# Kernel tuning notes

Hardware: AMD Instinct MI355X
Metric: run time of the kernel (lower is better)

Reference implementation:

```python
import jax, jax.numpy as jnp
import numpy as np

HIDDEN = 2048
B, T, K = 64, 512, 49  # K = 7x7 spatial grid

def setup_inputs() -> dict:
    key = jax.random.key(0)
    ks = jax.random.split(key, 7)
    def xavier(k, shape):
        fan_in, fan_out = shape[1], shape[0]
        bound = float(np.sqrt(6.0 / (fan_in + fan_out)))
        return jax.random.uniform(k, shape, jnp.float32, -bound, bound)
    return {
        "V": jax.random.normal(ks[0], (B, K, HIDDEN), jnp.float32),
        "h_t": jax.random.normal(ks[1], (B, T, HIDDEN), jnp.float32),
        "sent_t": jax.random.normal(ks[2], (B, T, HIDDEN), jnp.float32),
        "Wv": xavier(ks[3], (K, HIDDEN)),
        "Wg": xavier(ks[4], (K, HIDDEN)),
        "Ws": xavier(ks[5], (K, HIDDEN)),
        "Wh": xavier(ks[6], (1, K)),
    }

def reference(V, h_t, sent_t, Wv, Wg, Ws, Wh):
    # Dropout is identity (eval mode / deterministic reference).
    wh = Wh[0]                                    # [K]
    pv = jnp.einsum('bkd,jd->bkj', V, Wv)         # [B,K,K]
    pg = jnp.einsum('btd,jd->btj', h_t, Wg)       # [B,T,K]
    content_v = pv[:, None, :, :] + pg[:, :, None, :]   # [B,T,K,K]
    z_t = jnp.tanh(content_v) @ wh                # [B,T,K]
    alpha_t = jax.nn.softmax(z_t, axis=-1)        # spatial attention
    c_t = jnp.einsum('btk,bkd->btd', alpha_t, V)  # [B,T,HIDDEN]
    content_s = jnp.einsum('btd,jd->btj', sent_t, Ws) + pg  # [B,T,K]
    z_ext = jnp.tanh(content_s) @ wh              # [B,T]
    extend = jnp.concatenate([z_t, z_ext[..., None]], axis=-1)  # [B,T,K+1]
    alpha_hat = jax.nn.softmax(extend, axis=-1)
    beta_t = alpha_hat[:, :, -1:]                 # sentinel gate [B,T,1]
    c_hat_t = beta_t * sent_t + (1.0 - beta_t) * c_t
    return (c_hat_t, alpha_t, beta_t)
```

## Files before the change

### kernel.cpp

```cpp
#include <hip/hip_runtime.h>

#define HIDDEN 2048
#define NB 64
#define NT 512
#define NK 49

typedef __attribute__((ext_vector_type(4))) float f32x4;
typedef __attribute__((ext_vector_type(8))) short short8;

__device__ __forceinline__ unsigned cvtpk_bf16(float a, float b) {
    unsigned r;
    asm("v_cvt_pk_bf16_f32 %0, %1, %2" : "=v"(r) : "v"(a), "v"(b));
    return r;
}

__device__ __forceinline__ unsigned short f2bf(float x) {
    union { float f; unsigned u; } v; v.f = x;
    unsigned r = v.u + 0x7FFF + ((v.u >> 16) & 1);
    return (unsigned short)(r >> 16);
}

__global__ __launch_bounds__(256) void convert_w(
    const float* __restrict__ Wg, const float* __restrict__ Ws,
    const float* __restrict__ Wv, unsigned short* __restrict__ Wf)
{
    int tau = blockIdx.x * 256 + threadIdx.x;
    int m   = tau >> 14;
    int rem = tau & 16383;
    int c   = rem >> 12;
    int s   = (rem >> 6) & 63;
    int l   = rem & 63;
    int col = c * 16 + (l & 15);
    int k0  = s * 32 + ((l >> 4) << 3);

    const float* W = (m == 0) ? Wg : (m == 1) ? Ws : Wv;
    unsigned short out[8];
    if (col < NK) {
        const float* p = W + (size_t)col * HIDDEN + k0;
        #pragma unroll
        for (int j = 0; j < 8; j++) out[j] = f2bf(p[j]);
    } else {
        #pragma unroll
        for (int j = 0; j < 8; j++) out[j] = 0;
    }
    unsigned short* dst = Wf + (size_t)tau * 8;
    #pragma unroll
    for (int j = 0; j < 8; j++) dst[j] = out[j];
}

__global__ __launch_bounds__(256) void gemm_mfma(
    const float* __restrict__ h, const float* __restrict__ s,
    const float* __restrict__ V, const unsigned short* __restrict__ Wf,
    float* __restrict__ pg, float* __restrict__ ps, float* __restrict__ pv)
{
    int w = threadIdx.x >> 6, lane = threadIdx.x & 63;
    int gw = blockIdx.x * 4 + w;

    const float* A; float* C; int rowBase; const unsigned short* wf;
    if (gw < 2048)      { A = h; C = pg; rowBase = gw * 16;          wf = Wf; }
    else if (gw < 4096) { A = s; C = ps; rowBase = (gw - 2048) * 16; wf = Wf + (size_t)16384 * 8; }
    else                { A = V; C = pv; rowBase = (gw - 4096) * 16; wf = Wf + (size_t)32768 * 8; }

    const float* ap = A + (size_t)(rowBase + (lane & 15)) * HIDDEN + ((lane >> 4) << 3);
    const short8* bp = (const short8*)(wf + (size_t)lane * 8);

    f32x4 acc0 = {0.f, 0.f, 0.f, 0.f};
    f32x4 acc1 = acc0, acc2 = acc0, acc3 = acc0;

    #pragma unroll 2
    for (int st = 0; st < 64; st++) {
        float4 f0 = *(const float4*)(ap + st * 32);
        float4 f1 = *(const float4*)(ap + st * 32 + 4);

        union { short8 v; unsigned u[4]; } a;
        a.u[0] = cvtpk_bf16(f0.x, f0.y);
        a.u[1] = cvtpk_bf16(f0.z, f0.w);
        a.u[2] = cvtpk_bf16(f1.x, f1.y);
        a.u[3] = cvtpk_bf16(f1.z, f1.w);

        short8 b0 = bp[(0 * 64 + st) * 64];
        short8 b1 = bp[(1 * 64 + st) * 64];
        short8 b2 = bp[(2 * 64 + st) * 64];
        short8 b3 = bp[(3 * 64 + st) * 64];

        acc0 = __builtin_amdgcn_mfma_f32_16x16x32_bf16(a.v, b0, acc0, 0, 0, 0);
        acc1 = __builtin_amdgcn_mfma_f32_16x16x32_bf16(a.v, b1, acc1, 0, 0, 0);
        acc2 = __builtin_amdgcn_mfma_f32_16x16x32_bf16(a.v, b2, acc2, 0, 0, 0);
        acc3 = __builtin_amdgcn_mfma_f32_16x16x32_bf16(a.v, b3, acc3, 0, 0, 0);
    }

    int colb  = lane & 15;
    int rquad = (lane >> 4) << 2;
    float* crow = C + (size_t)(rowBase + rquad) * NK + colb;
    #pragma unroll
    for (int r = 0; r < 4; r++) {
        crow[(size_t)r * NK + 0]  = acc0[r];
        crow[(size_t)r * NK + 16] = acc1[r];
        crow[(size_t)r * NK + 32] = acc2[r];
    }
    if (colb == 0) {
        #pragma unroll
        for (int r = 0; r < 4; r++) crow[(size_t)r * NK + 48] = acc3[r];
    }
}

__device__ __forceinline__ float ftanh(float x) {
    float e = __expf(2.f * x);
    return 1.f - 2.f * __builtin_amdgcn_rcpf(e + 1.f);
}

__global__ __launch_bounds__(256) void zab_kernel(
    const float* __restrict__ pg, const float* __restrict__ ps,
    const float* __restrict__ pv, const float* __restrict__ Wh,
    float* __restrict__ alpha, float* __restrict__ beta)
{
    int w = threadIdx.x >> 6, lane = threadIdx.x & 63;
    int row = blockIdx.x * 4 + w;
    int b = row >> 9;

    const float* pgrow = pg + (size_t)row * NK;
    const float* psrow = ps + (size_t)row * NK;

    float va = 0.f;
    if (lane < NK)
        va = ftanh(psrow[lane] + pgrow[lane]) * Wh[lane];
    float z_ext = va;
    #pragma unroll
    for (int off = 32; off; off >>= 1) z_ext += __shfl_xor(z_ext, off);

    float z = -1e30f;
    if (lane < NK) {
        const float* pvrow = pv + ((size_t)b * NK + lane) * NK;
        float acc = 0.f;
        for (int j = 0; j < NK; j++)
            acc = fmaf(ftanh(pvrow[j] + pgrow[j]), Wh[j], acc);
        z = acc;
    }

    float m = z;
    #pragma unroll
    for (int off = 32; off; off >>= 1) m = fmaxf(m, __shfl_xor(m, off));
    float p = (lane < NK) ? __expf(z - m) : 0.f;
    float ssum = p;
    #pragma unroll
    for (int off = 32; off; off >>= 1) ssum += __shfl_xor(ssum, off);
    float a = p * __builtin_amdgcn_rcpf(ssum);

    if (lane < NK)
        alpha[(size_t)row * NK + lane] = a;

    float me = fmaxf(m, z_ext);
    float se = ssum * __expf(m - me) + __expf(z_ext - me);
    float bet = __expf(z_ext - me) * __builtin_amdgcn_rcpf(se);
    if (lane == 0) beta[row] = bet;
}

__global__ __launch_bounds__(256) void chat_kernel(
    const float* __restrict__ V, const float* __restrict__ sent,
    const float* __restrict__ alpha, const float* __restrict__ beta,
    float* __restrict__ chat)
{
    int d0 = blockIdx.x * 128;
    int t0 = blockIdx.y * 32;
    int b  = blockIdx.z;

    __shared__ float alpha_s[NK][36];
    __shared__ float beta_s[32];

    int tid = threadIdx.x;

    const float* arow = alpha + ((size_t)b * NT + t0) * NK;
    for (int i = tid; i < 32 * NK; i += 256) {
        int t = i / NK, k = i - t * NK;
        alpha_s[k][t] = arow[i];
    }
    if (tid < 32) beta_s[tid] = beta[(size_t)b * NT + t0 + tid];
    __syncthreads();

    int tx = tid & 31;
    int ty = tid >> 5;

    const float* vp = V + (size_t)b * NK * HIDDEN + d0 + tx * 4;

    float4 acc[4];
    #pragma unroll
    for (int i = 0; i < 4; i++) acc[i] = make_float4(0.f, 0.f, 0.f, 0.f);

    #pragma unroll 7
    for (int k = 0; k < NK; k++) {
        float4 vv = *(const float4*)(vp + (size_t)k * HIDDEN);
        float4 a4 = *(const float4*)&alpha_s[k][ty * 4];
        acc[0].x = fmaf(a4.x, vv.x, acc[0].x);
        acc[0].y = fmaf(a4.x, vv.y, acc[0].y);
        acc[0].z = fmaf(a4.x, vv.z, acc[0].z);
        acc[0].w = fmaf(a4.x, vv.w, acc[0].w);
        acc[1].x = fmaf(a4.y, vv.x, acc[1].x);
        acc[1].y = fmaf(a4.y, vv.y, acc[1].y);
        acc[1].z = fmaf(a4.y, vv.z, acc[1].z);
        acc[1].w = fmaf(a4.y, vv.w, acc[1].w);
        acc[2].x = fmaf(a4.z, vv.x, acc[2].x);
        acc[2].y = fmaf(a4.z, vv.y, acc[2].y);
        acc[2].z = fmaf(a4.z, vv.z, acc[2].z);
        acc[2].w = fmaf(a4.z, vv.w, acc[2].w);
        acc[3].x = fmaf(a4.w, vv.x, acc[3].x);
        acc[3].y = fmaf(a4.w, vv.y, acc[3].y);
        acc[3].z = fmaf(a4.w, vv.z, acc[3].z);
        acc[3].w = fmaf(a4.w, vv.w, acc[3].w);
    }

    #pragma unroll
    for (int i = 0; i < 4; i++) {
        int t = ty * 4 + i;
        float bt = beta_s[t];
        const float* sp = sent + ((size_t)b * NT + t0 + t) * HIDDEN + d0 + tx * 4;
        float*       op = chat + ((size_t)b * NT + t0 + t) * HIDDEN + d0 + tx * 4;
        float4 sv = *(const float4*)sp;
        float4 o;
        o.x = fmaf(bt, sv.x, (1.f - bt) * acc[i].x);
        o.y = fmaf(bt, sv.y, (1.f - bt) * acc[i].y);
        o.z = fmaf(bt, sv.z, (1.f - bt) * acc[i].z);
        o.w = fmaf(bt, sv.w, (1.f - bt) * acc[i].w);
        *(float4*)op = o;
    }
}

extern "C" void kernel_launch(void* const* d_in, const int* in_sizes, int n_in,
                              void* d_out, int out_size, void* d_ws, size_t ws_size,
                              hipStream_t stream)
{
    const float* V    = (const float*)d_in[0];
    const float* h_t  = (const float*)d_in[1];
    const float* sent = (const float*)d_in[2];
    const float* Wv   = (const float*)d_in[3];
    const float* Wg   = (const float*)d_in[4];
    const float* Ws   = (const float*)d_in[5];
    const float* Wh   = (const float*)d_in[6];

    float* out   = (float*)d_out;
    float* chat  = out;
    float* alpha = out + (size_t)NB * NT * HIDDEN;
    float* beta  = alpha + (size_t)NB * NT * NK;

    float* ws = (float*)d_ws;
    float* pg = ws;
    float* ps = pg + (size_t)NB * NT * NK;
    float* pv = ps + (size_t)NB * NT * NK;
    unsigned short* Wf = (unsigned short*)(pv + (size_t)NB * NK * NK);

    convert_w<<<192, 256, 0, stream>>>(Wg, Ws, Wv, Wf);
    gemm_mfma<<<1073, 256, 0, stream>>>(h_t, sent, V, Wf, pg, ps, pv);
    zab_kernel<<<(NB * NT) / 4, 256, 0, stream>>>(pg, ps, pv, Wh, alpha, beta);
    chat_kernel<<<dim3(HIDDEN / 128, NT / 32, NB), 256, 0, stream>>>(V, sent, alpha, beta, chat);
}
```

Measured before the change: 387.0 us.

## Share weight tiles across waves via double-buffered LDS in MFMA GEMM

The projection GEMM now stages the bf16 weight fragments in shared memory, so the four waves of a block share one global read of each weight chunk instead of each wave re-reading every chunk from cache. The weight staging is double-buffered, and the fp32 activation rows are prefetched several k-steps ahead in registers to overlap loads with MFMA work. The weight-conversion kernel's output layout is reordered so each k-chunk is contiguous. This adds per-chunk block barriers, more registers and LDS usage, which can reduce occupancy.

Result: faster. 351.7 us (-9.1%).

```diff
diff --git a/kernel.cpp b/kernel.cpp
--- a/kernel.cpp
+++ b/kernel.cpp
@@ -27,11 +27,11 @@
     int tau = blockIdx.x * 256 + threadIdx.x;
     int m   = tau >> 14;
     int rem = tau & 16383;
-    int c   = rem >> 12;
-    int s   = (rem >> 6) & 63;
+    int st  = rem >> 8;
+    int c   = (rem >> 6) & 3;
     int l   = rem & 63;
     int col = c * 16 + (l & 15);
-    int k0  = s * 32 + ((l >> 4) << 3);
+    int k0  = st * 32 + ((l >> 4) << 3);
 
     const float* W = (m == 0) ? Wg : (m == 1) ? Ws : Wv;
     unsigned short out[8];
@@ -54,44 +54,91 @@
     float* __restrict__ pg, float* __restrict__ ps, float* __restrict__ pv)
 {
     int w = threadIdx.x >> 6, lane = threadIdx.x & 63;
-    int gw = blockIdx.x * 4 + w;
-
-    const float* A; float* C; int rowBase; const unsigned short* wf;
-    if (gw < 2048)      { A = h; C = pg; rowBase = gw * 16;          wf = Wf; }
-    else if (gw < 4096) { A = s; C = ps; rowBase = (gw - 2048) * 16; wf = Wf + (size_t)16384 * 8; }
-    else                { A = V; C = pv; rowBase = (gw - 4096) * 16; wf = Wf + (size_t)32768 * 8; }
-
-    const float* ap = A + (size_t)(rowBase + (lane & 15)) * HIDDEN + ((lane >> 4) << 3);
-    const short8* bp = (const short8*)(wf + (size_t)lane * 8);
+    int blk = blockIdx.x;
+
+    const float* A; float* C; int rowBase; const unsigned short* wfm;
+    if (blk < 512)       { A = h; C = pg; rowBase = blk * 64;          wfm = Wf; }
+    else if (blk < 1024) { A = s; C = ps; rowBase = (blk - 512) * 64;  wfm = Wf + (size_t)16384 * 8; }
+    else                 { A = V; C = pv; rowBase = (blk - 1024) * 64; wfm = Wf + (size_t)32768 * 8; }
+
+    const float* ap = A + (size_t)(rowBase + w * 16 + (lane & 15)) * HIDDEN + ((lane >> 4) << 3);
+    const short8* wfp = (const short8*)wfm;
+
+    __shared__ short8 lb[2][1024];
+    short8* lbp0 = &lb[0][0];
+    short8* lbp1 = &lb[1][0];
+    int q = w * 4;
 
     f32x4 acc0 = {0.f, 0.f, 0.f, 0.f};
     f32x4 acc1 = acc0, acc2 = acc0, acc3 = acc0;
 
-    #pragma unroll 2
-    for (int st = 0; st < 64; st++) {
-        float4 f0 = *(const float4*)(ap + st * 32);
-        float4 f1 = *(const float4*)(ap + st * 32 + 4);
-
-        union { short8 v; unsigned u[4]; } a;
-        a.u[0] = cvtpk_bf16(f0.x, f0.y);
-        a.u[1] = cvtpk_bf16(f0.z, f0.w);
-        a.u[2] = cvtpk_bf16(f1.x, f1.y);
-        a.u[3] = cvtpk_bf16(f1.z, f1.w);
-
-        short8 b0 = bp[(0 * 64 + st) * 64];
-        short8 b1 = bp[(1 * 64 + st) * 64];
-        short8 b2 = bp[(2 * 64 + st) * 64];
-        short8 b3 = bp[(3 * 64 + st) * 64];
-
-        acc0 = __builtin_amdgcn_mfma_f32_16x16x32_bf16(a.v, b0, acc0, 0, 0, 0);
-        acc1 = __builtin_amdgcn_mfma_f32_16x16x32_bf16(a.v, b1, acc1, 0, 0, 0);
-        acc2 = __builtin_amdgcn_mfma_f32_16x16x32_bf16(a.v, b2, acc2, 0, 0, 0);
-        acc3 = __builtin_amdgcn_mfma_f32_16x16x32_bf16(a.v, b3, acc3, 0, 0, 0);
-    }
+    float4 a0_0, a0_1, a1_0, a1_1, a2_0, a2_1, a3_0, a3_1;
+    short8 bs0, bs1, bs2, bs3;
+
+#define LOADBS(ch) { \
+    bs0 = wfp[(ch) * 1024 + (q + 0) * 64 + lane]; \
+    bs1 = wfp[(ch) * 1024 + (q + 1) * 64 + lane]; \
+    bs2 = wfp[(ch) * 1024 + (q + 2) * 64 + lane]; \
+    bs3 = wfp[(ch) * 1024 + (q + 3) * 64 + lane]; }
+
+#define WRITEBS(lbp) { \
+    lbp[(q + 0) * 64 + lane] = bs0; \
+    lbp[(q + 1) * 64 + lane] = bs1; \
+    lbp[(q + 2) * 64 + lane] = bs2; \
+    lbp[(q + 3) * 64 + lane] = bs3; }
+
+#define LOADA2(A0, A1, gst) { \
+    A0 = *(const float4*)(ap + (gst) * 32); \
+    A1 = *(const float4*)(ap + (gst) * 32 + 4); }
+
+#define STEP(lbp, sti, Aa, Ab, rgst, dorf) { \
+    union { short8 v; unsigned u[4]; } a_; \
+    a_.u[0] = cvtpk_bf16(Aa.x, Aa.y); \
+    a_.u[1] = cvtpk_bf16(Aa.z, Aa.w); \
+    a_.u[2] = cvtpk_bf16(Ab.x, Ab.y); \
+    a_.u[3] = cvtpk_bf16(Ab.z, Ab.w); \
+    short8 b0 = lbp[((sti) * 4 + 0) * 64 + lane]; \
+    short8 b1 = lbp[((sti) * 4 + 1) * 64 + lane]; \
+    short8 b2 = lbp[((sti) * 4 + 2) * 64 + lane]; \
+    short8 b3 = lbp[((sti) * 4 + 3) * 64 + lane]; \
+    if (dorf) { LOADA2(Aa, Ab, rgst) } \
+    acc0 = __builtin_amdgcn_mfma_f32_16x16x32_bf16(a_.v, b0, acc0, 0, 0, 0); \
+    acc1 = __builtin_amdgcn_mfma_f32_16x16x32_bf16(a_.v, b1, acc1, 0, 0, 0); \
+    acc2 = __builtin_amdgcn_mfma_f32_16x16x32_bf16(a_.v, b2, acc2, 0, 0, 0); \
+    acc3 = __builtin_amdgcn_mfma_f32_16x16x32_bf16(a_.v, b3, acc3, 0, 0, 0); }
+
+    LOADBS(0)
+    LOADA2(a0_0, a0_1, 0)
+    LOADA2(a1_0, a1_1, 1)
+    LOADA2(a2_0, a2_1, 2)
+    LOADA2(a3_0, a3_1, 3)
+    WRITEBS(lbp0)
+    LOADBS(1)
+    __syncthreads();
+
+    #pragma unroll 1
+    for (int ch = 0; ch < 16; ch++) {
+        short8* cur = (ch & 1) ? lbp1 : lbp0;
+        short8* nxt = (ch & 1) ? lbp0 : lbp1;
+        if (ch < 15) { WRITEBS(nxt) }
+        if (ch < 14) { LOADBS(ch + 2) }
+        bool rf = ch < 15;
+        int g = (ch + 1) * 4;
+        STEP(cur, 0, a0_0, a0_1, g + 0, rf)
+        STEP(cur, 1, a1_0, a1_1, g + 1, rf)
+        STEP(cur, 2, a2_0, a2_1, g + 2, rf)
+        STEP(cur, 3, a3_0, a3_1, g + 3, rf)
+        __syncthreads();
+    }
+
+#undef LOADBS
+#undef WRITEBS
+#undef LOADA2
+#undef STEP
 
     int colb  = lane & 15;
     int rquad = (lane >> 4) << 2;
-    float* crow = C + (size_t)(rowBase + rquad) * NK + colb;
+    float* crow = C + (size_t)(rowBase + w * 16 + rquad) * NK + colb;
     #pragma unroll
     for (int r = 0; r < 4; r++) {
         crow[(size_t)r * NK + 0]  = acc0[r];
```

## Software-pipeline GEMM loads with triple-buffered inline-asm prefetch and interleaved weight layout

Applied to the files above, without the earlier changes.

Rewrites the MFMA GEMM main loop as a three-stage software pipeline. Each step issues raw global_load_dwordx4 instructions for the A and B fragments several steps ahead and waits with explicit vmcnt counters, so memory latency overlaps with the MFMAs. The prepacked bf16 weight layout is reordered so the four column tiles for a given k-step sit next to each other, letting one base pointer with immediate offsets fetch all four. This costs more registers and depends on hand-placed waitcnt being correct, and clamped redundant loads at the tail add some extra traffic.

Result: faster. 377.8 us (-2.4%).

```diff
diff --git a/kernel.cpp b/kernel.cpp
--- a/kernel.cpp
+++ b/kernel.cpp
@@ -27,11 +27,11 @@
     int tau = blockIdx.x * 256 + threadIdx.x;
     int m   = tau >> 14;
     int rem = tau & 16383;
-    int c   = rem >> 12;
-    int s   = (rem >> 6) & 63;
+    int st  = rem >> 8;
+    int c   = (rem >> 6) & 3;
     int l   = rem & 63;
     int col = c * 16 + (l & 15);
-    int k0  = s * 32 + ((l >> 4) << 3);
+    int k0  = st * 32 + ((l >> 4) << 3);
 
     const float* W = (m == 0) ? Wg : (m == 1) ? Ws : Wv;
     unsigned short out[8];
@@ -48,6 +48,30 @@
     for (int j = 0; j < 8; j++) dst[j] = out[j];
 }
 
+#define ISSUE6(Aa, Ab, B0, B1, B2, B3, g) { \
+    int gc_ = (g) < 64 ? (g) : 63; \
+    const float*  _pa = ap + (size_t)gc_ * 32; \
+    const short8* _pb = bp + (size_t)gc_ * 256; \
+    asm volatile("global_load_dwordx4 %0, %1, off"             : "=&v"(Aa) : "v"(_pa)); \
+    asm volatile("global_load_dwordx4 %0, %1, off offset:16"   : "=&v"(Ab) : "v"(_pa)); \
+    asm volatile("global_load_dwordx4 %0, %1, off"             : "=&v"(B0) : "v"(_pb)); \
+    asm volatile("global_load_dwordx4 %0, %1, off offset:1024" : "=&v"(B1) : "v"(_pb)); \
+    asm volatile("global_load_dwordx4 %0, %1, off offset:2048" : "=&v"(B2) : "v"(_pb)); \
+    asm volatile("global_load_dwordx4 %0, %1, off offset:3072" : "=&v"(B3) : "v"(_pb)); }
+
+#define CONSUME(Aa, Ab, B0, B1, B2, B3) { \
+    asm volatile("s_waitcnt vmcnt(12)" ::: "memory"); \
+    __builtin_amdgcn_sched_barrier(0); \
+    union { short8 v; unsigned u[4]; } a_; \
+    a_.u[0] = cvtpk_bf16(Aa[0], Aa[1]); \
+    a_.u[1] = cvtpk_bf16(Aa[2], Aa[3]); \
+    a_.u[2] = cvtpk_bf16(Ab[0], Ab[1]); \
+    a_.u[3] = cvtpk_bf16(Ab[2], Ab[3]); \
+    acc0 = __builtin_amdgcn_mfma_f32_16x16x32_bf16(a_.v, B0, acc0, 0, 0, 0); \
+    acc1 = __builtin_amdgcn_mfma_f32_16x16x32_bf16(a_.v, B1, acc1, 0, 0, 0); \
+    acc2 = __builtin_amdgcn_mfma_f32_16x16x32_bf16(a_.v, B2, acc2, 0, 0, 0); \
+    acc3 = __builtin_amdgcn_mfma_f32_16x16x32_bf16(a_.v, B3, acc3, 0, 0, 0); }
+
 __global__ __launch_bounds__(256) void gemm_mfma(
     const float* __restrict__ h, const float* __restrict__ s,
     const float* __restrict__ V, const unsigned short* __restrict__ Wf,
@@ -56,38 +80,37 @@
     int w = threadIdx.x >> 6, lane = threadIdx.x & 63;
     int gw = blockIdx.x * 4 + w;
 
-    const float* A; float* C; int rowBase; const unsigned short* wf;
-    if (gw < 2048)      { A = h; C = pg; rowBase = gw * 16;          wf = Wf; }
-    else if (gw < 4096) { A = s; C = ps; rowBase = (gw - 2048) * 16; wf = Wf + (size_t)16384 * 8; }
-    else                { A = V; C = pv; rowBase = (gw - 4096) * 16; wf = Wf + (size_t)32768 * 8; }
+    const float* A; float* C; int rowBase; const unsigned short* wfm;
+    if (gw < 2048)      { A = h; C = pg; rowBase = gw * 16;          wfm = Wf; }
+    else if (gw < 4096) { A = s; C = ps; rowBase = (gw - 2048) * 16; wfm = Wf + (size_t)16384 * 8; }
+    else                { A = V; C = pv; rowBase = (gw - 4096) * 16; wfm = Wf + (size_t)32768 * 8; }
 
     const float* ap = A + (size_t)(rowBase + (lane & 15)) * HIDDEN + ((lane >> 4) << 3);
-    const short8* bp = (const short8*)(wf + (size_t)lane * 8);
+    const short8* bp = (const short8*)wfm + lane;
 
     f32x4 acc0 = {0.f, 0.f, 0.f, 0.f};
     f32x4 acc1 = acc0, acc2 = acc0, acc3 = acc0;
 
-    #pragma unroll 2
-    for (int st = 0; st < 64; st++) {
-        float4 f0 = *(const float4*)(ap + st * 32);
-        float4 f1 = *(const float4*)(ap + st * 32 + 4);
-
-        union { short8 v; unsigned u[4]; } a;
-        a.u[0] = cvtpk_bf16(f0.x, f0.y);
-        a.u[1] = cvtpk_bf16(f0.z, f0.w);
-        a.u[2] = cvtpk_bf16(f1.x, f1.y);
-        a.u[3] = cvtpk_bf16(f1.z, f1.w);
-
-        short8 b0 = bp[(0 * 64 + st) * 64];
-        short8 b1 = bp[(1 * 64 + st) * 64];
-        short8 b2 = bp[(2 * 64 + st) * 64];
-        short8 b3 = bp[(3 * 64 + st) * 64];
-
-        acc0 = __builtin_amdgcn_mfma_f32_16x16x32_bf16(a.v, b0, acc0, 0, 0, 0);
-        acc1 = __builtin_amdgcn_mfma_f32_16x16x32_bf16(a.v, b1, acc1, 0, 0, 0);
-        acc2 = __builtin_amdgcn_mfma_f32_16x16x32_bf16(a.v, b2, acc2, 0, 0, 0);
-        acc3 = __builtin_amdgcn_mfma_f32_16x16x32_bf16(a.v, b3, acc3, 0, 0, 0);
-    }
+    f32x4 A0a, A0b, A1a, A1b, A2a, A2b;
+    short8 B00, B01, B02, B03, B10, B11, B12, B13, B20, B21, B22, B23;
+
+    ISSUE6(A0a, A0b, B00, B01, B02, B03, 0)
+    ISSUE6(A1a, A1b, B10, B11, B12, B13, 1)
+    ISSUE6(A2a, A2b, B20, B21, B22, B23, 2)
+
+    #pragma unroll 1
+    for (int g = 0; g < 63; g += 3) {
+        CONSUME(A0a, A0b, B00, B01, B02, B03)
+        ISSUE6 (A0a, A0b, B00, B01, B02, B03, g + 3)
+        CONSUME(A1a, A1b, B10, B11, B12, B13)
+        ISSUE6 (A1a, A1b, B10, B11, B12, B13, g + 4)
+        CONSUME(A2a, A2b, B20, B21, B22, B23)
+        ISSUE6 (A2a, A2b, B20, B21, B22, B23, g + 5)
+    }
+    CONSUME(A0a, A0b, B00, B01, B02, B03)
+
+    asm volatile("s_waitcnt vmcnt(0)" ::: "memory");
+    __builtin_amdgcn_sched_barrier(0);
 
     int colb  = lane & 15;
     int rquad = (lane >> 4) << 2;
```

## Stage GEMM tiles in LDS with double-buffered async global-to-LDS loads

Applied to the files above, without the earlier changes.

The projection GEMM now works on 128-row block tiles with 8 waves. A and the packed bf16 weights are staged into shared memory through global_load_lds in a double-buffered 64-wide K loop, and the A tile uses an XOR swizzle. The weight packing is reordered so each K chunk is contiguous. Each block loads the weights once instead of every wave fetching them separately, and the async copy is meant to overlap with the MFMA work. The cost is a barrier per chunk, more LDS (which limits occupancy), and row clamping plus a masked store for the partial V tile.

After: 358.3 us. -7.4%, faster.

```diff
diff --git a/kernel.cpp b/kernel.cpp
--- a/kernel.cpp
+++ b/kernel.cpp
@@ -5,6 +5,10 @@
 #define NT 512
 #define NK 49
 
+#define BM 128
+#define BK 64
+#define NCH (HIDDEN/BK)
+
 typedef __attribute__((ext_vector_type(4))) float f32x4;
 typedef __attribute__((ext_vector_type(8))) short short8;
 
@@ -27,11 +31,11 @@
     int tau = blockIdx.x * 256 + threadIdx.x;
     int m   = tau >> 14;
     int rem = tau & 16383;
-    int c   = rem >> 12;
-    int s   = (rem >> 6) & 63;
+    int st  = rem >> 8;
+    int c   = (rem >> 6) & 3;
     int l   = rem & 63;
     int col = c * 16 + (l & 15);
-    int k0  = s * 32 + ((l >> 4) << 3);
+    int k0  = st * 32 + ((l >> 4) << 3);
 
     const float* W = (m == 0) ? Wg : (m == 1) ? Ws : Wv;
     unsigned short out[8];
@@ -48,59 +52,93 @@
     for (int j = 0; j < 8; j++) dst[j] = out[j];
 }
 
-__global__ __launch_bounds__(256) void gemm_mfma(
+__global__ __launch_bounds__(512) void gemm_mfma(
     const float* __restrict__ h, const float* __restrict__ s,
     const float* __restrict__ V, const unsigned short* __restrict__ Wf,
     float* __restrict__ pg, float* __restrict__ ps, float* __restrict__ pv)
 {
-    int w = threadIdx.x >> 6, lane = threadIdx.x & 63;
-    int gw = blockIdx.x * 4 + w;
-
-    const float* A; float* C; int rowBase; const unsigned short* wf;
-    if (gw < 2048)      { A = h; C = pg; rowBase = gw * 16;          wf = Wf; }
-    else if (gw < 4096) { A = s; C = ps; rowBase = (gw - 2048) * 16; wf = Wf + (size_t)16384 * 8; }
-    else                { A = V; C = pv; rowBase = (gw - 4096) * 16; wf = Wf + (size_t)32768 * 8; }
-
-    const float* ap = A + (size_t)(rowBase + (lane & 15)) * HIDDEN + ((lane >> 4) << 3);
-    const short8* bp = (const short8*)(wf + (size_t)lane * 8);
+    int tid = threadIdx.x;
+    int w = tid >> 6, lane = tid & 63;
+    int blk = blockIdx.x;
+
+    const float* A; float* C; int rowBase; const unsigned short* wfm; int Mrows;
+    if (blk < 256)      { A = h; C = pg; rowBase = blk * BM;         wfm = Wf;                       Mrows = 32768; }
+    else if (blk < 512) { A = s; C = ps; rowBase = (blk - 256) * BM; wfm = Wf + (size_t)16384 * 8;   Mrows = 32768; }
+    else                { A = V; C = pv; rowBase = (blk - 512) * BM; wfm = Wf + (size_t)32768 * 8;   Mrows = 3136;  }
+
+    __shared__ float  Alds[2][BM * BK];
+    __shared__ short8 Blds[2][512];
+
+    const short8* wfp = (const short8*)wfm;
+    int rt0 = w * 16;
 
     f32x4 acc0 = {0.f, 0.f, 0.f, 0.f};
     f32x4 acc1 = acc0, acc2 = acc0, acc3 = acc0;
 
-    #pragma unroll 2
-    for (int st = 0; st < 64; st++) {
-        float4 f0 = *(const float4*)(ap + st * 32);
-        float4 f1 = *(const float4*)(ap + st * 32 + 4);
-
-        union { short8 v; unsigned u[4]; } a;
-        a.u[0] = cvtpk_bf16(f0.x, f0.y);
-        a.u[1] = cvtpk_bf16(f0.z, f0.w);
-        a.u[2] = cvtpk_bf16(f1.x, f1.y);
-        a.u[3] = cvtpk_bf16(f1.z, f1.w);
-
-        short8 b0 = bp[(0 * 64 + st) * 64];
-        short8 b1 = bp[(1 * 64 + st) * 64];
-        short8 b2 = bp[(2 * 64 + st) * 64];
-        short8 b3 = bp[(3 * 64 + st) * 64];
-
-        acc0 = __builtin_amdgcn_mfma_f32_16x16x32_bf16(a.v, b0, acc0, 0, 0, 0);
-        acc1 = __builtin_amdgcn_mfma_f32_16x16x32_bf16(a.v, b1, acc1, 0, 0, 0);
-        acc2 = __builtin_amdgcn_mfma_f32_16x16x32_bf16(a.v, b2, acc2, 0, 0, 0);
-        acc3 = __builtin_amdgcn_mfma_f32_16x16x32_bf16(a.v, b3, acc3, 0, 0, 0);
-    }
+#define DMA_AB(ch, buf) { \
+    _Pragma("unroll") \
+    for (int i = 0; i < 4; i++) { \
+        int rt = rt0 + i * 4 + (lane >> 4); \
+        int gr = rowBase + rt; if (gr > Mrows - 1) gr = Mrows - 1; \
+        int sg = (lane & 15) ^ (rt & 7); \
+        const float* src = A + (size_t)gr * HIDDEN + (ch) * BK + sg * 4; \
+        __builtin_amdgcn_global_load_lds((const void*)src, \
+            (void*)&Alds[buf][(rt0 + i * 4) * BK], 16, 0, 0); \
+    } \
+    { const short8* srcb = wfp + (size_t)((ch) * 8 + w) * 64 + lane; \
+      __builtin_amdgcn_global_load_lds((const void*)srcb, \
+          (void*)&Blds[buf][w * 64], 16, 0, 0); } }
+
+#define CHUNK_COMPUTE(buf) { \
+    const float*  al = &Alds[buf][0]; \
+    const short8* bl = &Blds[buf][0]; \
+    int rr = lane & 15; \
+    int row = rt0 + rr; \
+    _Pragma("unroll") \
+    for (int st = 0; st < 2; st++) { \
+        int cs = st * 8 + ((lane >> 4) << 1); \
+        float4 f0 = *(const float4*)&al[row * BK + ((cs    ) ^ (rr & 7)) * 4]; \
+        float4 f1 = *(const float4*)&al[row * BK + ((cs + 1) ^ (rr & 7)) * 4]; \
+        union { short8 v; unsigned u[4]; } a_; \
+        a_.u[0] = cvtpk_bf16(f0.x, f0.y); \
+        a_.u[1] = cvtpk_bf16(f0.z, f0.w); \
+        a_.u[2] = cvtpk_bf16(f1.x, f1.y); \
+        a_.u[3] = cvtpk_bf16(f1.z, f1.w); \
+        short8 b0 = bl[(st * 4 + 0) * 64 + lane]; \
+        short8 b1 = bl[(st * 4 + 1) * 64 + lane]; \
+        short8 b2 = bl[(st * 4 + 2) * 64 + lane]; \
+        short8 b3 = bl[(st * 4 + 3) * 64 + lane]; \
+        acc0 = __builtin_amdgcn_mfma_f32_16x16x32_bf16(a_.v, b0, acc0, 0, 0, 0); \
+        acc1 = __builtin_amdgcn_mfma_f32_16x16x32_bf16(a_.v, b1, acc1, 0, 0, 0); \
+        acc2 = __builtin_amdgcn_mfma_f32_16x16x32_bf16(a_.v, b2, acc2, 0, 0, 0); \
+        acc3 = __builtin_amdgcn_mfma_f32_16x16x32_bf16(a_.v, b3, acc3, 0, 0, 0); \
+    } }
+
+    DMA_AB(0, 0)
+
+    #pragma unroll 1
+    for (int ch = 0; ch < NCH; ch++) {
+        int cur = ch & 1;
+        __syncthreads();
+        if (ch + 1 < NCH) { DMA_AB(ch + 1, cur ^ 1) }
+        CHUNK_COMPUTE(cur)
+    }
+
+#undef DMA_AB
+#undef CHUNK_COMPUTE
 
     int colb  = lane & 15;
     int rquad = (lane >> 4) << 2;
-    float* crow = C + (size_t)(rowBase + rquad) * NK + colb;
+    int rowb  = rowBase + rt0 + rquad;
+    float* crow = C + (size_t)rowb * NK + colb;
     #pragma unroll
     for (int r = 0; r < 4; r++) {
-        crow[(size_t)r * NK + 0]  = acc0[r];
-        crow[(size_t)r * NK + 16] = acc1[r];
-        crow[(size_t)r * NK + 32] = acc2[r];
-    }
-    if (colb == 0) {
-        #pragma unroll
-        for (int r = 0; r < 4; r++) crow[(size_t)r * NK + 48] = acc3[r];
+        if (rowb + r < Mrows) {
+            crow[(size_t)r * NK + 0]  = acc0[r];
+            crow[(size_t)r * NK + 16] = acc1[r];
+            crow[(size_t)r * NK + 32] = acc2[r];
+            if (colb == 0) crow[(size_t)r * NK + 48] = acc3[r];
+        }
     }
 }
 
@@ -248,7 +286,7 @@
     unsigned short* Wf = (unsigned short*)(pv + (size_t)NB * NK * NK);
 
     convert_w<<<192, 256, 0, stream>>>(Wg, Ws, Wv, Wf);
-    gemm_mfma<<<1073, 256, 0, stream>>>(h_t, sent, V, Wf, pg, ps, pv);
+    gemm_mfma<<<537, 512, 0, stream>>>(h_t, sent, V, Wf, pg, ps, pv);
     zab_kernel<<<(NB * NT) / 4, 256, 0, stream>>>(pg, ps, pv, Wh, alpha, beta);
     chat_kernel<<<dim3(HIDDEN / 128, NT / 32, NB), 256, 0, stream>>>(V, sent, alpha, beta, chat);
 }
```
